# Kernel tuning notes

Measured on AMD Instinct MI355X. Metric: run time of the kernel, lower is better.

## Reference

```python
import jax, jax.numpy as jnp
import numpy as np

NUM_LABELS = 51  # labels 0..50; label 0 = background, excluded from loss
EPS = 1e-8

def setup_inputs() -> dict:
    key = jax.random.key(0)
    k1, k2 = jax.random.split(key)
    prediction = jax.random.normal(k1, (2, 16, 32, 256, 256), dtype=jnp.float32)
    gt = jax.random.randint(k2, (2, 32, 256, 256), 0, NUM_LABELS, dtype=jnp.int64)
    return {"prediction": prediction, "gt": gt}

def reference(prediction, gt):
    b, c, z, y, x = prediction.shape
    L1 = NUM_LABELS  # number of segments (incl. background 0)
    # batchwise: channels first, flatten all voxels -> (N, c)
    p = jnp.transpose(prediction, (1, 0, 2, 3, 4)).reshape(c, -1).T  # (N, c)
    ids = gt.reshape(-1).astype(jnp.int32)                           # (N,)
    ones = jnp.ones_like(ids, dtype=p.dtype)
    counts = jax.ops.segment_sum(ones, ids, num_segments=L1)         # (L1,)
    sums = jax.ops.segment_sum(p, ids, num_segments=L1)              # (L1, c)
    means = sums / jnp.maximum(counts, 1.0)[:, None]                 # (L1, c)
    # intra: per-voxel cosine with its label's mean vector, averaged per label
    m_vox = means[ids]                                               # (N, c)
    dot = jnp.sum(p * m_vox, axis=1)                                 # (N,)
    pn = jnp.linalg.norm(p, axis=1)
    mn = jnp.linalg.norm(means, axis=1)[ids]
    cos = dot / jnp.maximum(pn * mn, EPS)
    intra_sum = jax.ops.segment_sum(cos, ids, num_segments=L1)
    intra_per_label = intra_sum[1:] / jnp.maximum(counts[1:], 1.0)   # exclude label 0
    intra_similarity = jnp.mean(intra_per_label)
    # inter: pairwise cosine between center means (labels 1..L)
    cm = means[1:]                                                   # (L, c)
    cmn = cm / jnp.maximum(jnp.linalg.norm(cm, axis=1, keepdims=True), EPS)
    G = cmn @ cmn.T                                                  # (L, L)
    iu, ju = jnp.triu_indices(L1 - 1, k=1)
    inter_similarities = G[iu, ju]
    clipped_inter = jnp.mean(jnp.clip(inter_similarities, 0.0, 1.0))
    # uniform_emb=False, dynamic_balancing=False, regularize=False
    loss = clipped_inter - intra_similarity
    return loss
```

## Files before the change

kernel.cpp:

```cpp
#include <hip/hip_runtime.h>


#define NL   51
#define SROW 33
#define NREP 4
#define TAB  (NREP * NL * SROW)

__global__ __launch_bounds__(256) void cl_pass1(const float* __restrict__ pred,
                                                const int*   __restrict__ gt,
                                                float* __restrict__ gtab) {
    __shared__ float tab[TAB];
    for (int i = threadIdx.x; i < TAB; i += 256) tab[i] = 0.f;
    __syncthreads();

    const unsigned tid  = threadIdx.x;
    const unsigned rep  = tid & (NREP - 1);
    const unsigned base = blockIdx.x * 4096u;

    #pragma unroll 1
    for (int k = 0; k < 16; ++k) {
        unsigned n    = base + k * 256u + tid;
        unsigned bidx = n >> 21;
        unsigned sp   = n & ((1u << 21) - 1);
        const float* pb = pred + ((size_t)bidx << 25) + sp;

        float v[16];
        float ss = 0.f;
        #pragma unroll
        for (int c = 0; c < 16; ++c) {
            v[c] = pb[(size_t)c << 21];
            ss += v[c] * v[c];
        }
        int   id = gt[n];
        float rn = (ss > 0.f) ? rsqrtf(ss) : 0.f;

        float* row = &tab[(rep * NL + (unsigned)id) * SROW];
        #pragma unroll
        for (int c = 0; c < 16; ++c) unsafeAtomicAdd(&row[c], v[c]);
        #pragma unroll
        for (int c = 0; c < 16; ++c) unsafeAtomicAdd(&row[16 + c], v[c] * rn);
        unsafeAtomicAdd(&row[32], 1.f);
    }
    __syncthreads();

    for (int i = threadIdx.x; i < NL * SROW; i += 256) {
        float t = tab[i] + tab[NL*SROW + i] + tab[2*NL*SROW + i] + tab[3*NL*SROW + i];
        unsafeAtomicAdd(&gtab[i], t);
    }
}

__global__ __launch_bounds__(256) void cl_final(const float* __restrict__ gtab,
                                                float* __restrict__ out) {
    __shared__ float means[NL][16];
    __shared__ float mn[NL];
    __shared__ float cnt[NL];
    __shared__ float cmn[NL - 1][16];
    __shared__ float red[256];
    __shared__ float intra_s;
    const int t = threadIdx.x;

    if (t < NL) cnt[t] = gtab[t * SROW + 32];
    __syncthreads();

    for (int i = t; i < NL * 16; i += 256) {
        int l = i >> 4, c = i & 15;
        means[l][c] = gtab[l * SROW + c] / fmaxf(cnt[l], 1.0f);
    }
    __syncthreads();

    if (t < NL) {
        float s = 0.f;
        #pragma unroll
        for (int c = 0; c < 16; ++c) s += means[t][c] * means[t][c];
        mn[t] = sqrtf(s);
    }
    __syncthreads();

    float intra = 0.f;
    if (t < NL - 1) {
        int l = t + 1;
        float d = 0.f;
        #pragma unroll
        for (int c = 0; c < 16; ++c) d += gtab[l * SROW + 16 + c] * means[l][c];
        float isum = (mn[l] > 0.f) ? d / mn[l] : 0.f;
        intra = isum / fmaxf(cnt[l], 1.0f);
    }
    red[t] = intra;
    __syncthreads();
    for (int s = 128; s > 0; s >>= 1) { if (t < s) red[t] += red[t + s]; __syncthreads(); }
    if (t == 0) intra_s = red[0] / (float)(NL - 1);

    for (int i = t; i < (NL - 1) * 16; i += 256) {
        int l = (i >> 4) + 1, c = i & 15;
        cmn[i >> 4][c] = means[l][c] / fmaxf(mn[l], 1e-8f);
    }
    __syncthreads();

    float acc = 0.f;
    int k = 0;
    for (int i = 0; i < NL - 2; ++i)
        for (int j = i + 1; j < NL - 1; ++j) {
            if ((k & 255) == t) {
                float d = 0.f;
                #pragma unroll
                for (int c = 0; c < 16; ++c) d += cmn[i][c] * cmn[j][c];
                acc += fminf(fmaxf(d, 0.f), 1.f);
            }
            ++k;
        }
    red[t] = acc;
    __syncthreads();
    for (int s = 128; s > 0; s >>= 1) { if (t < s) red[t] += red[t + s]; __syncthreads(); }
    if (t == 0) out[0] = red[0] / 1225.f - intra_s;
}

extern "C" void kernel_launch(void* const* d_in, const int* in_sizes, int n_in,
                              void* d_out, int out_size, void* d_ws, size_t ws_size,
                              hipStream_t stream) {
    const float* pred = (const float*)d_in[0];
    const int*   gt   = (const int*)d_in[1];
    float* gtab = (float*)d_ws;

    hipMemsetAsync(gtab, 0, NL * SROW * sizeof(float), stream);
    cl_pass1<<<1024, 256, 0, stream>>>(pred, gt, gtab);
    cl_final<<<1, 256, 0, stream>>>(gtab, (float*)d_out);
}
```

Baseline: 1.033 ms.

## Unroll voxel loop by two, use workgroup-scope LDS atomics, double grid

```diff
diff --git a/kernel.cpp b/kernel.cpp
--- a/kernel.cpp
+++ b/kernel.cpp
@@ -5,6 +5,9 @@
 #define SROW 33
 #define NREP 4
 #define TAB  (NREP * NL * SROW)
+
+#define LDSADD(idx, val) \
+    __hip_atomic_fetch_add(&tab[idx], (val), __ATOMIC_RELAXED, __HIP_MEMORY_SCOPE_WORKGROUP)
 
 __global__ __launch_bounds__(256) void cl_pass1(const float* __restrict__ pred,
                                                 const int*   __restrict__ gt,
@@ -15,31 +18,48 @@
 
     const unsigned tid  = threadIdx.x;
     const unsigned rep  = tid & (NREP - 1);
-    const unsigned base = blockIdx.x * 4096u;
+    const unsigned base = blockIdx.x * 2048u;
 
-    #pragma unroll 1
-    for (int k = 0; k < 16; ++k) {
-        unsigned n    = base + k * 256u + tid;
-        unsigned bidx = n >> 21;
-        unsigned sp   = n & ((1u << 21) - 1);
-        const float* pb = pred + ((size_t)bidx << 25) + sp;
+    for (int k = 0; k < 8; k += 2) {
+        unsigned nA = base + (unsigned)(k + 0) * 256u + tid;
+        unsigned nB = base + (unsigned)(k + 1) * 256u + tid;
+        const float* pA = pred + ((size_t)(nA >> 21) << 25) + (nA & 0x1FFFFFu);
+        const float* pB = pred + ((size_t)(nB >> 21) << 25) + (nB & 0x1FFFFFu);
 
-        float v[16];
-        float ss = 0.f;
+        float vA[16], vB[16];
         #pragma unroll
-        for (int c = 0; c < 16; ++c) {
-            v[c] = pb[(size_t)c << 21];
-            ss += v[c] * v[c];
+        for (int c = 0; c < 16; ++c) vA[c] = pA[(size_t)c << 21];
+        #pragma unroll
+        for (int c = 0; c < 16; ++c) vB[c] = pB[(size_t)c << 21];
+        int idA = gt[nA];
+        int idB = gt[nB];
+
+        float ssA = 0.f, ssB = 0.f;
+        #pragma unroll
+        for (int c = 0; c < 16; ++c) ssA += vA[c] * vA[c];
+        #pragma unroll
+        for (int c = 0; c < 16; ++c) ssB += vB[c] * vB[c];
+        float rnA = (ssA > 0.f) ? rsqrtf(ssA) : 0.f;
+        float rnB = (ssB > 0.f) ? rsqrtf(ssB) : 0.f;
+
+        {
+            unsigned row = (rep * NL + (unsigned)idA) * SROW;
+            #pragma unroll
+            for (int c = 0; c < 16; ++c) {
+                LDSADD(row + c,      vA[c]);
+                LDSADD(row + 16 + c, vA[c] * rnA);
+            }
+            LDSADD(row + 32, 1.f);
         }
-        int   id = gt[n];
-        float rn = (ss > 0.f) ? rsqrtf(ss) : 0.f;
-
-        float* row = &tab[(rep * NL + (unsigned)id) * SROW];
-        #pragma unroll
-        for (int c = 0; c < 16; ++c) unsafeAtomicAdd(&row[c], v[c]);
-        #pragma unroll
-        for (int c = 0; c < 16; ++c) unsafeAtomicAdd(&row[16 + c], v[c] * rn);
-        unsafeAtomicAdd(&row[32], 1.f);
+        {
+            unsigned row = (rep * NL + (unsigned)idB) * SROW;
+            #pragma unroll
+            for (int c = 0; c < 16; ++c) {
+                LDSADD(row + c,      vB[c]);
+                LDSADD(row + 16 + c, vB[c] * rnB);
+            }
+            LDSADD(row + 32, 1.f);
+        }
     }
     __syncthreads();
 
@@ -122,6 +142,6 @@
     float* gtab = (float*)d_ws;
 
     hipMemsetAsync(gtab, 0, NL * SROW * sizeof(float), stream);
-    cl_pass1<<<1024, 256, 0, stream>>>(pred, gt, gtab);
+    cl_pass1<<<2048, 256, 0, stream>>>(pred, gt, gtab);
     cl_final<<<1, 256, 0, stream>>>(gtab, (float*)d_out);
 }
```

After: 1.044 ms. Within noise of the previous version (+1.1%).
